# Optimization experiments

Measured on AMD Instinct MI355X. Metric: run time of the kernel, lower is better.

Reference implementation:

```python
import jax, jax.numpy as jnp
import numpy as np

N_PHENO = 50000
N_GENE = 50000
H = 128
N_LAYERS = 3  # num_layers=2 hidden convs + 1 final conv


def _seg_mean(x_src, edge, n_dst):
    # mean aggregation of source features onto destination nodes (PyG SAGEConv default)
    msg = x_src[edge[0]]                       # [E, H] gather
    s = jax.ops.segment_sum(msg, edge[1], num_segments=n_dst)
    cnt = jax.ops.segment_sum(jnp.ones((edge.shape[1],), x_src.dtype), edge[1], num_segments=n_dst)
    return s / jnp.maximum(cnt, 1.0)[:, None]


def _sage(x_src, x_dst, edge, Wl, bl, Wr, n_dst):
    # SAGEConv: lin_l(mean_j x_j) + lin_r(x_i); lin_l has bias, lin_r does not
    return _seg_mean(x_src, edge, n_dst) @ Wl + bl + x_dst @ Wr


def setup_inputs() -> dict:
    key = jax.random.key(0)
    ks = jax.random.split(key, 16)
    d = {
        'x_pheno': jax.random.normal(ks[0], (N_PHENO, H), jnp.float32),
        'x_gene': jax.random.normal(ks[1], (N_GENE, H), jnp.float32),
    }
    scale = 1.0 / np.sqrt(H)
    names = ['Wl_isa', 'bl_isa', 'Wr_isa', 'Wl_rel', 'bl_rel', 'Wr_rel', 'Wl_rev', 'bl_rev', 'Wr_rev']
    for i, nm in enumerate(names):
        shp = (N_LAYERS, H) if nm.startswith('b') else (N_LAYERS, H, H)
        d[nm] = jax.random.normal(ks[2 + i], shp, jnp.float32) * scale
    d['edge_isa'] = jax.random.randint(ks[11], (2, 500000), 0, N_PHENO, jnp.int64)
    d['edge_rel'] = jax.random.randint(ks[12], (2, 1000000), 0, N_GENE, jnp.int64)
    d['edge_rev'] = jax.random.randint(ks[13], (2, 1000000), 0, N_PHENO, jnp.int64)
    d['edge_label_index'] = jax.random.randint(ks[14], (2, 500000), 0, N_PHENO, jnp.int64)
    return d


def reference(x_pheno, x_gene, Wl_isa, bl_isa, Wr_isa, Wl_rel, bl_rel, Wr_rel,
              Wl_rev, bl_rev, Wr_rev, edge_isa, edge_rel, edge_rev, edge_label_index):
    xp, xg = x_pheno, x_gene
    n_p, n_g = xp.shape[0], xg.shape[0]
    for i in range(N_LAYERS):
        # HeteroConv aggr='sum': sum SAGE outputs across edge types per dst node type
        new_p = (_sage(xp, xp, edge_isa, Wl_isa[i], bl_isa[i], Wr_isa[i], n_p)
                 + _sage(xg, xp, edge_rev, Wl_rev[i], bl_rev[i], Wr_rev[i], n_p))
        new_g = _sage(xp, xg, edge_rel, Wl_rel[i], bl_rel[i], Wr_rel[i], n_g)
        if i < N_LAYERS - 1:  # leaky_relu after hidden convs, not after `final`
            new_p = jax.nn.leaky_relu(new_p, 0.01)
            new_g = jax.nn.leaky_relu(new_g, 0.01)
        xp, xg = new_p, new_g
    # Classifier: dot-product edge decoder + sigmoid
    score = (xp[edge_label_index[0]] * xg[edge_label_index[1]]).sum(axis=-1)
    return jax.nn.sigmoid(score)
```

## Files before the change

kernel.cpp:

```cpp
#include <hip/hip_runtime.h>
#include <hip/hip_bf16.h>
#include <math.h>

#define H 128
#define RS 136
#define BSH 9
#define BINW 512
#define BCAP 11264
#define KEDGE 4096
#define EPT 16
#define MAXBINS 1024

typedef __attribute__((ext_vector_type(8))) short short8;
typedef __attribute__((ext_vector_type(4))) short short4v;
typedef __attribute__((ext_vector_type(4))) float f32x4;
typedef __attribute__((ext_vector_type(2))) _Float16 half2v;
typedef __attribute__((ext_vector_type(4))) _Float16 half4v;
typedef __attribute__((ext_vector_type(8))) _Float16 half8v;

__device__ __forceinline__ short f2bf(float f) {
    unsigned u = __float_as_uint(f);
    u += 0x7fff + ((u >> 16) & 1);
    return (short)(u >> 16);
}
__device__ __forceinline__ float bf2f(short h) {
    return __uint_as_float(((unsigned)(unsigned short)h) << 16);
}


__global__ __launch_bounds__(256) void bin_count_kernel(
    const int* __restrict__ e0, int E0, const int* __restrict__ e1, int E1,
    const int* __restrict__ e2, int E2, int* __restrict__ bin_tot,
    int NPn, int NGn, int nbins, int E_tot) {
    __shared__ int hist[MAXBINS];
    int t = threadIdx.x;
    for (int i = t; i < nbins; i += 256) hist[i] = 0;
    __syncthreads();
    int base_e = blockIdx.x * KEDGE;
#pragma unroll
    for (int j = 0; j < EPT; ++j) {
        int g = base_e + j * 256 + t;
        if (g < E_tot) {
            const int* ed; int E, lo, nbase;
            if (g < E0) { ed = e0; E = E0; lo = g; nbase = 0; }
            else if (g < E0 + E1) { ed = e1; E = E1; lo = g - E0; nbase = NPn; }
            else { ed = e2; E = E2; lo = g - E0 - E1; nbase = NPn + NGn; }
            int gdst = nbase + ed[E + lo];
            atomicAdd(&hist[gdst >> BSH], 1);
        }
    }
    __syncthreads();
    for (int i = t; i < nbins; i += 256) {
        int h = hist[i];
        if (h) atomicAdd(&bin_tot[i * 16], h);
    }
}

__global__ __launch_bounds__(1024) void scan_bins(const int* __restrict__ bin_tot, int nbins,
                                                  int* __restrict__ bin_base,
                                                  int* __restrict__ bin_cur) {
    __shared__ int sh[1024];
    int t = threadIdx.x;
    int v = (t < nbins) ? bin_tot[t * 16] : 0;
    sh[t] = v;
    __syncthreads();
    for (int off = 1; off < 1024; off <<= 1) {
        int u = (t >= off) ? sh[t - off] : 0;
        __syncthreads();
        sh[t] += u;
        __syncthreads();
    }
    if (t < nbins) {
        int ex = sh[t] - v;
        bin_base[t] = ex;
        bin_cur[t * 16] = ex;
    }
    if (t == nbins - 1) bin_base[nbins] = sh[t];
}

__global__ __launch_bounds__(256) void bin_scatter_kernel(
    const int* __restrict__ e0, int E0, const int* __restrict__ e1, int E1,
    const int* __restrict__ e2, int E2, int* __restrict__ bin_cur,
    int* __restrict__ temp, int NPn, int NGn, int nbins, int E_tot) {
    __shared__ int hist[MAXBINS];
    __shared__ int cur[MAXBINS];
    int t = threadIdx.x;
    for (int i = t; i < nbins; i += 256) hist[i] = 0;
    __syncthreads();
    int vals[EPT], bins[EPT];
    int base_e = blockIdx.x * KEDGE;
#pragma unroll
    for (int j = 0; j < EPT; ++j) {
        int g = base_e + j * 256 + t;
        int b = -1, v = 0;
        if (g < E_tot) {
            const int* ed; int E, lo, nbase;
            if (g < E0) { ed = e0; E = E0; lo = g; nbase = 0; }
            else if (g < E0 + E1) { ed = e1; E = E1; lo = g - E0; nbase = NPn; }
            else { ed = e2; E = E2; lo = g - E0 - E1; nbase = NPn + NGn; }
            int src = ed[lo];
            int gdst = nbase + ed[E + lo];
            v = src | ((gdst & (BINW - 1)) << 16);
            b = gdst >> BSH;
            atomicAdd(&hist[b], 1);
        }
        vals[j] = v;
        bins[j] = b;
    }
    __syncthreads();
    for (int i = t; i < nbins; i += 256) {
        int h = hist[i];
        cur[i] = h ? atomicAdd(&bin_cur[i * 16], h) : 0;
    }
    __syncthreads();
#pragma unroll
    for (int j = 0; j < EPT; ++j) {
        if (bins[j] >= 0) {
            int p = atomicAdd(&cur[bins[j]], 1);
            temp[p] = vals[j];
        }
    }
}

__global__ __launch_bounds__(256) void bin_sort_kernel(
    const int* __restrict__ bin_base, const int* __restrict__ temp,
    int* __restrict__ col, int* __restrict__ rowptr, int n_tot, int nbins) {
    __shared__ int srt[BCAP];
    __shared__ int cur[BINW];
    __shared__ int pfx[BINW];
    __shared__ int red[256];
    int b = blockIdx.x;
    int start = b << BSH;
    int nodes = n_tot - start; if (nodes > BINW) nodes = BINW;
    int t = threadIdx.x;
    int base = bin_base[b];
    int count = bin_base[b + 1] - base;
    for (int i = t; i < BINW; i += 256) cur[i] = 0;
    __syncthreads();
    for (int i = t; i < count; i += 256)
        atomicAdd(&cur[(temp[base + i] >> 16) & (BINW - 1)], 1);
    __syncthreads();
    int a0 = cur[2 * t], a1 = cur[2 * t + 1];
    red[t] = a0 + a1;
    __syncthreads();
    for (int off = 1; off < 256; off <<= 1) {
        int u = (t >= off) ? red[t - off] : 0;
        __syncthreads();
        red[t] += u;
        __syncthreads();
    }
    int excl = red[t] - (a0 + a1);
    pfx[2 * t] = excl;
    pfx[2 * t + 1] = excl + a0;
    __syncthreads();
    for (int i = t; i < nodes; i += 256) rowptr[start + i] = base + pfx[i];
    if (b == nbins - 1 && t == 0) rowptr[n_tot] = base + count;
    for (int i = t; i < BINW; i += 256) cur[i] = pfx[i];
    __syncthreads();
    if (count <= BCAP) {
        for (int i = t; i < count; i += 256) {
            int v = temp[base + i];
            int p = atomicAdd(&cur[(v >> 16) & (BINW - 1)], 1);
            srt[p] = v & 0xFFFF;
        }
        __syncthreads();
        for (int i = t; i < count; i += 256) col[base + i] = srt[i];
    } else {
        for (int i = t; i < count; i += 256) {
            int v = temp[base + i];
            int p = atomicAdd(&cur[(v >> 16) & (BINW - 1)], 1);
            col[base + p] = v & 0xFFFF;
        }
    }
}


struct WSrc { const float* a[15]; const float* b[15]; };

__global__ __launch_bounds__(256) void pack_w_kernel(WSrc src, short* __restrict__ whi,
                                                     short* __restrict__ wlo) {
    int idx = blockIdx.x * 256 + threadIdx.x;
    if (idx >= 15 * 4 * 8 * 64) return;
    int lane = idx & 63;
    int ct = (idx >> 6) & 7;
    int kc = (idx >> 9) & 3;
    int mat = idx >> 11;
    const float* A = src.a[mat];
    const float* Bp = src.b[mat];
    int n = ct * 16 + (lane & 15);
    int kbase = kc * 32 + (lane >> 4) * 8;
    size_t o = (size_t)idx * 8;
    for (int j = 0; j < 8; ++j) {
        float v = A[(size_t)(kbase + j) * H + n];
        if (Bp) v += Bp[(size_t)(kbase + j) * H + n];
        short h = f2bf(v);
        whi[o + j] = h;
        wlo[o + j] = f2bf(v - bf2f(h));
    }
}


__global__ __launch_bounds__(256) void cvt16_kernel(const float* __restrict__ x,
                                                    _Float16* __restrict__ y, int n4) {
    int i = blockIdx.x * 256 + threadIdx.x;
    if (i >= n4) return;
    f32x4 v = *(const f32x4*)&x[(size_t)i * 4];
    half4v h;
#pragma unroll
    for (int k = 0; k < 4; ++k) h[k] = (_Float16)v[k];
    *(half4v*)&y[(size_t)i * 4] = h;
}


__device__ __forceinline__ float2 seg16(const _Float16* __restrict__ x,
                                        const int* __restrict__ col,
                                        int beg, int end, int voff) {
    float ax0 = 0.f, ax1 = 0.f, ax2 = 0.f, ax3 = 0.f;
    float ay0 = 0.f, ay1 = 0.f, ay2 = 0.f, ay3 = 0.f;
    int e = beg;
    while (e + 16 <= end) {
        half2v v[16];
#pragma unroll
        for (int i = 0; i < 16; ++i) {
            int si = __builtin_amdgcn_readfirstlane(col[e + i]);
            v[i] = *(const half2v*)(x + (size_t)si * H + voff);
        }
#pragma unroll
        for (int i = 0; i < 16; i += 4) {
            ax0 += (float)v[i + 0][0]; ay0 += (float)v[i + 0][1];
            ax1 += (float)v[i + 1][0]; ay1 += (float)v[i + 1][1];
            ax2 += (float)v[i + 2][0]; ay2 += (float)v[i + 2][1];
            ax3 += (float)v[i + 3][0]; ay3 += (float)v[i + 3][1];
        }
        e += 16;
    }
    int rem = end - e;
    if (rem > 0) {
        int last = end - 1;
        half2v v[16];
#pragma unroll
        for (int i = 0; i < 16; ++i) {
            int p = e + i; if (p > last) p = last;
            int si = __builtin_amdgcn_readfirstlane(col[p]);
            v[i] = *(const half2v*)(x + (size_t)si * H + voff);
        }
#pragma unroll
        for (int i = 0; i < 16; ++i) {
            float m = (i < rem) ? 1.0f : 0.0f;
            float fx = (float)v[i][0], fy = (float)v[i][1];
            if ((i & 3) == 0) { ax0 = fmaf(fx, m, ax0); ay0 = fmaf(fy, m, ay0); }
            else if ((i & 3) == 1) { ax1 = fmaf(fx, m, ax1); ay1 = fmaf(fy, m, ay1); }
            else if ((i & 3) == 2) { ax2 = fmaf(fx, m, ax2); ay2 = fmaf(fy, m, ay2); }
            else { ax3 = fmaf(fx, m, ax3); ay3 = fmaf(fy, m, ay3); }
        }
    }
    float sx = (ax0 + ax1) + (ax2 + ax3);
    float sy = (ay0 + ay1) + (ay2 + ay3);
    int c = end - beg; if (c < 1) c = 1;
    float inv = 1.0f / (float)c;
    return (float2){sx * inv, sy * inv};
}

__global__ __launch_bounds__(256) void agg_all_kernel(
    const _Float16* __restrict__ xp, const _Float16* __restrict__ xg,
    const int* __restrict__ rowptr, const int* __restrict__ col,
    float* __restrict__ M1, float* __restrict__ M2, float* __restrict__ M3,
    int NPn, int NGn) {
    int wl = __builtin_amdgcn_readfirstlane((int)threadIdx.x >> 6);
    int w = (blockIdx.x << 2) + wl;
    int lane = threadIdx.x & 63;
    int voff = lane * 2;
    if (w < NPn) {
        float2 r1 = seg16(xp, col, rowptr[w], rowptr[w + 1], voff);
        *(float2*)&M1[(size_t)w * H + voff] = r1;
        int b = NPn + NGn + w;
        float2 r2 = seg16(xg, col, rowptr[b], rowptr[b + 1], voff);
        *(float2*)&M2[(size_t)w * H + voff] = r2;
    } else if (w < NPn + NGn) {
        float2 r3 = seg16(xp, col, rowptr[w], rowptr[w + 1], voff);
        *(float2*)&M3[(size_t)(w - NPn) * H + voff] = r3;
    }
}


struct GIn { const float* f; const short* hi; const short* lo; };

template <int NIN>
__global__ __launch_bounds__(256, 3) void gemm_mfma(
    GIn a0, GIn a1, GIn a2,
    const short* __restrict__ whi, const short* __restrict__ wlo,
    int mat0, int mat1, int mat2,
    const float* __restrict__ b0, const float* __restrict__ b1,
    _Float16* __restrict__ out16, short* __restrict__ ohi, short* __restrict__ olo,
    int n_rows, int relu) {
    __shared__ short Ahi[64 * RS];
    __shared__ short Alo[64 * RS];
    const int tid = threadIdx.x;
    const int lane = tid & 63;
    const int wave = tid >> 6;
    const int r0 = blockIdx.x * 64;
    const int ct0 = wave * 2;
    const int m16 = lane & 15;
    const int acol = (lane >> 4) * 8;

    f32x4 acc[4][2];
#pragma unroll
    for (int mt = 0; mt < 4; ++mt)
#pragma unroll
        for (int c = 0; c < 2; ++c) acc[mt][c] = (f32x4){0.f, 0.f, 0.f, 0.f};

    const GIn ins[3] = {a0, a1, a2};
    const int marr[3] = {mat0, mat1, mat2};

    short8 bh[2][2], bl[2][2];
    {
        const short* wh = whi + (size_t)marr[0] * (H * H);
        const short* wl = wlo + (size_t)marr[0] * (H * H);
        size_t f0 = ((size_t)ct0 * 64 + lane) * 8;
        bh[0][0] = *(const short8*)&wh[f0];
        bh[0][1] = *(const short8*)&wh[f0 + 512];
        bl[0][0] = *(const short8*)&wl[f0];
        bl[0][1] = *(const short8*)&wl[f0 + 512];
    }

#pragma unroll
    for (int m = 0; m < NIN; ++m) {
        const short* __restrict__ wh = whi + (size_t)marr[m] * (H * H);
        const short* __restrict__ wl = wlo + (size_t)marr[m] * (H * H);
        __syncthreads();
        if (ins[m].hi) {
#pragma unroll
            for (int i = 0; i < 8; ++i) {
                int f = tid + i * 256;
                int row = f >> 5;
                int c4 = (f & 31) * 4;
                int gr = r0 + row;
                if (gr >= n_rows) gr = n_rows - 1;
                size_t o = (size_t)gr * H + c4;
                *(short4v*)&Ahi[row * RS + c4] = *(const short4v*)&ins[m].hi[o];
                *(short4v*)&Alo[row * RS + c4] = *(const short4v*)&ins[m].lo[o];
            }
        } else {
            const float* __restrict__ A = ins[m].f;
#pragma unroll
            for (int i = 0; i < 8; ++i) {
                int f = tid + i * 256;
                int row = f >> 5;
                int c4 = (f & 31) * 4;
                int gr = r0 + row;
                if (gr >= n_rows) gr = n_rows - 1;
                float4 v = *(const float4*)&A[(size_t)gr * H + c4];
                short h0 = f2bf(v.x), h1 = f2bf(v.y), h2 = f2bf(v.z), h3 = f2bf(v.w);
                *(short4v*)&Ahi[row * RS + c4] = (short4v){h0, h1, h2, h3};
                *(short4v*)&Alo[row * RS + c4] =
                    (short4v){f2bf(v.x - bf2f(h0)), f2bf(v.y - bf2f(h1)),
                              f2bf(v.z - bf2f(h2)), f2bf(v.w - bf2f(h3))};
            }
        }
        __syncthreads();
#pragma unroll
        for (int kc = 0; kc < 4; ++kc) {
            if (kc < 3) {
                int nb = (kc + 1) & 1;
                size_t f = ((size_t)((kc + 1) * 8 + ct0) * 64 + lane) * 8;
                bh[nb][0] = *(const short8*)&wh[f];
                bh[nb][1] = *(const short8*)&wh[f + 512];
                bl[nb][0] = *(const short8*)&wl[f];
                bl[nb][1] = *(const short8*)&wl[f + 512];
            } else if (m + 1 < NIN) {
                const short* wh2 = whi + (size_t)marr[m + 1] * (H * H);
                const short* wl2 = wlo + (size_t)marr[m + 1] * (H * H);
                size_t f = ((size_t)ct0 * 64 + lane) * 8;
                bh[0][0] = *(const short8*)&wh2[f];
                bh[0][1] = *(const short8*)&wh2[f + 512];
                bl[0][0] = *(const short8*)&wl2[f];
                bl[0][1] = *(const short8*)&wl2[f + 512];
            }
            int cb = kc & 1;
#pragma unroll
            for (int mt = 0; mt < 4; ++mt) {
                short8 ah = *(const short8*)&Ahi[(mt * 16 + m16) * RS + kc * 32 + acol];
                short8 al = *(const short8*)&Alo[(mt * 16 + m16) * RS + kc * 32 + acol];
#pragma unroll
                for (int c = 0; c < 2; ++c) {
                    acc[mt][c] = __builtin_amdgcn_mfma_f32_16x16x32_bf16(ah, bh[cb][c], acc[mt][c], 0, 0, 0);
                    acc[mt][c] = __builtin_amdgcn_mfma_f32_16x16x32_bf16(al, bh[cb][c], acc[mt][c], 0, 0, 0);
                    acc[mt][c] = __builtin_amdgcn_mfma_f32_16x16x32_bf16(ah, bl[cb][c], acc[mt][c], 0, 0, 0);
                }
            }
        }
    }

    const int rquad = (lane >> 4) * 4;
    const int ncol = lane & 15;
#pragma unroll
    for (int c = 0; c < 2; ++c) {
        int n = (ct0 + c) * 16 + ncol;
        float bs = b0[n];
        if (b1) bs += b1[n];
#pragma unroll
        for (int mt = 0; mt < 4; ++mt) {
#pragma unroll
            for (int reg = 0; reg < 4; ++reg) {
                int gr = r0 + mt * 16 + rquad + reg;
                if (gr < n_rows) {
                    float v = acc[mt][c][reg] + bs;
                    if (relu) v = v > 0.f ? v : 0.01f * v;
                    size_t o = (size_t)gr * H + n;
                    out16[o] = (_Float16)v;
                    short h = f2bf(v);
                    ohi[o] = h;
                    olo[o] = f2bf(v - bf2f(h));
                }
            }
        }
    }
}


__global__ __launch_bounds__(256) void scores_kernel(const _Float16* __restrict__ xp,
                                                     const _Float16* __restrict__ xg,
                                                     const int* __restrict__ eli, int E,
                                                     float* __restrict__ out) {
    int lane16 = threadIdx.x & 15;
    int sub = threadIdx.x >> 4;
    int e = blockIdx.x * 16 + sub;
    if (e >= E) return;
    int ip = eli[e];
    int ig = eli[E + e];
    half8v a = *(const half8v*)&xp[(size_t)ip * H + lane16 * 8];
    half8v b = *(const half8v*)&xg[(size_t)ig * H + lane16 * 8];
    float s = 0.f;
#pragma unroll
    for (int k = 0; k < 8; ++k) s += (float)a[k] * (float)b[k];
#pragma unroll
    for (int off = 8; off; off >>= 1) s += __shfl_xor(s, off, 16);
    if (lane16 == 0) out[e] = 1.0f / (1.0f + expf(-s));
}


extern "C" void kernel_launch(void* const* d_in, const int* in_sizes, int n_in,
                              void* d_out, int out_size, void* d_ws, size_t ws_size,
                              hipStream_t stream) {
    const float* x_pheno = (const float*)d_in[0];
    const float* x_gene  = (const float*)d_in[1];
    const float* Wl_isa  = (const float*)d_in[2];
    const float* bl_isa  = (const float*)d_in[3];
    const float* Wr_isa  = (const float*)d_in[4];
    const float* Wl_rel  = (const float*)d_in[5];
    const float* bl_rel  = (const float*)d_in[6];
    const float* Wr_rel  = (const float*)d_in[7];
    const float* Wl_rev  = (const float*)d_in[8];
    const float* bl_rev  = (const float*)d_in[9];
    const float* Wr_rev  = (const float*)d_in[10];
    const int* e_isa = (const int*)d_in[11];
    const int* e_rel = (const int*)d_in[12];
    const int* e_rev = (const int*)d_in[13];
    const int* e_lbl = (const int*)d_in[14];
    const int E_isa = in_sizes[11] / 2;
    const int E_rel = in_sizes[12] / 2;
    const int E_rev = in_sizes[13] / 2;
    const int E_lbl = in_sizes[14] / 2;
    const int NP = in_sizes[0] / H;
    const int NG = in_sizes[1] / H;
    const int NMAX = NP > NG ? NP : NG;
    const int n_tot = NP + NG + NP;
    const int E_tot = E_isa + E_rel + E_rev;
    const int nbins = (n_tot + BINW - 1) / BINW;

    char* ws = (char*)d_ws;
    auto alloc = [&](size_t bytes) -> char* {
        char* p = ws;
        ws += (bytes + 255) & ~(size_t)255;
        return p;
    };
    float* M1 = (float*)alloc((size_t)NMAX * H * sizeof(float));
    float* M2 = (float*)alloc((size_t)NMAX * H * sizeof(float));
    float* M3 = (float*)alloc((size_t)NMAX * H * sizeof(float));
    int* rowptr  = (int*)alloc((size_t)(n_tot + 1) * 4);
    int* col     = (int*)alloc((size_t)E_tot * 4);
    int* temp    = (int*)alloc((size_t)E_tot * 4);
    int* bin_tot = (int*)alloc((size_t)nbins * 16 * 4);
    int* bin_cur = (int*)alloc((size_t)nbins * 16 * 4);
    int* bin_base= (int*)alloc((size_t)(nbins + 1) * 4);
    short* whi = (short*)alloc((size_t)15 * H * H * sizeof(short));
    short* wlo = (short*)alloc((size_t)15 * H * H * sizeof(short));
    _Float16* xp16 = (_Float16*)alloc((size_t)NP * H * sizeof(_Float16));
    _Float16* xg16 = (_Float16*)alloc((size_t)NG * H * sizeof(_Float16));
    short* xph = (short*)alloc((size_t)NP * H * sizeof(short));
    short* xpl = (short*)alloc((size_t)NP * H * sizeof(short));
    short* xgh = (short*)alloc((size_t)NG * H * sizeof(short));
    short* xgl = (short*)alloc((size_t)NG * H * sizeof(short));

    hipMemsetAsync(bin_tot, 0, (size_t)nbins * 16 * 4, stream);
    bin_count_kernel<<<(E_tot + KEDGE - 1) / KEDGE, 256, 0, stream>>>(
        e_isa, E_isa, e_rel, E_rel, e_rev, E_rev, bin_tot, NP, NG, nbins, E_tot);
    scan_bins<<<1, 1024, 0, stream>>>(bin_tot, nbins, bin_base, bin_cur);
    bin_scatter_kernel<<<(E_tot + KEDGE - 1) / KEDGE, 256, 0, stream>>>(
        e_isa, E_isa, e_rel, E_rel, e_rev, E_rev, bin_cur, temp, NP, NG, nbins, E_tot);
    bin_sort_kernel<<<nbins, 256, 0, stream>>>(bin_base, temp, col, rowptr, n_tot, nbins);

    WSrc src;
    for (int l = 0; l < 3; ++l) {
        src.a[l * 5 + 0] = Wl_isa + (size_t)l * H * H;  src.b[l * 5 + 0] = nullptr;
        src.a[l * 5 + 1] = Wl_rev + (size_t)l * H * H;  src.b[l * 5 + 1] = nullptr;
        src.a[l * 5 + 2] = Wr_isa + (size_t)l * H * H;  src.b[l * 5 + 2] = Wr_rev + (size_t)l * H * H;
        src.a[l * 5 + 3] = Wl_rel + (size_t)l * H * H;  src.b[l * 5 + 3] = nullptr;
        src.a[l * 5 + 4] = Wr_rel + (size_t)l * H * H;  src.b[l * 5 + 4] = nullptr;
    }
    pack_w_kernel<<<(15 * 4 * 8 * 64 + 255) / 256, 256, 0, stream>>>(src, whi, wlo);

    cvt16_kernel<<<(NP * H / 4 + 255) / 256, 256, 0, stream>>>(x_pheno, xp16, NP * H / 4);
    cvt16_kernel<<<(NG * H / 4 + 255) / 256, 256, 0, stream>>>(x_gene, xg16, NG * H / 4);

    const short *pph = nullptr, *ppl = nullptr, *pgh = nullptr, *pgl = nullptr;
    for (int l = 0; l < 3; ++l) {
        agg_all_kernel<<<(NP + NG + 3) / 4, 256, 0, stream>>>(
            xp16, xg16, rowptr, col, M1, M2, M3, NP, NG);
        int relu = (l < 2) ? 1 : 0;
        const float* bli = bl_isa + (size_t)l * H;
        const float* blv = bl_rev + (size_t)l * H;
        const float* blr = bl_rel + (size_t)l * H;
        GIn a0{M1, nullptr, nullptr};
        GIn a1{M2, nullptr, nullptr};
        GIn a2{l == 0 ? x_pheno : nullptr, pph, ppl};
        gemm_mfma<3><<<(NP + 63) / 64, 256, 0, stream>>>(
            a0, a1, a2, whi, wlo, l * 5 + 0, l * 5 + 1, l * 5 + 2, bli, blv,
            xp16, xph, xpl, NP, relu);
        GIn g0{M3, nullptr, nullptr};
        GIn g1{l == 0 ? x_gene : nullptr, pgh, pgl};
        GIn g2{nullptr, nullptr, nullptr};
        gemm_mfma<2><<<(NG + 63) / 64, 256, 0, stream>>>(
            g0, g1, g2, whi, wlo, l * 5 + 3, l * 5 + 4, 0, blr, nullptr,
            xg16, xgh, xgl, NG, relu);
        pph = xph; ppl = xpl; pgh = xgh; pgl = xgl;
    }

    scores_kernel<<<(E_lbl + 15) / 16, 256, 0, stream>>>(xp16, xg16, e_lbl, E_lbl, (float*)d_out);
}
```

Baseline: 669.8 us.

## Fuse neighbor aggregation into GEMM and drop separate bin-count pass

Mean aggregation now runs inside the MFMA GEMM kernel: each block gathers its 64 rows directly into shared-memory bf16 hi/lo tiles, which removes the fp32 M1/M2/M3 intermediates and their global write and read-back. Because aggregation now reads the fp16 features while new features are written, the fp16 buffers are double-buffered across layers. CSR construction drops the separate counting pass by scattering into fixed-capacity per-bin slots and scanning afterwards; edges beyond the slot capacity would be silently dropped. The two input conversions are merged into one launch and a short-tail path is added to the segment gather. The fused kernel puts irregular gather latency in front of the MFMA work and no longer prefetches the next weight tile.

```diff
diff --git a/kernel.cpp b/kernel.cpp
--- a/kernel.cpp
+++ b/kernel.cpp
@@ -7,12 +7,14 @@
 #define BSH 9
 #define BINW 512
 #define BCAP 11264
+#define BSLOT 12288
 #define KEDGE 4096
 #define EPT 16
 #define MAXBINS 1024
 
 typedef __attribute__((ext_vector_type(8))) short short8;
 typedef __attribute__((ext_vector_type(4))) short short4v;
+typedef __attribute__((ext_vector_type(2))) short short2v;
 typedef __attribute__((ext_vector_type(4))) float f32x4;
 typedef __attribute__((ext_vector_type(2))) _Float16 half2v;
 typedef __attribute__((ext_vector_type(4))) _Float16 half4v;
@@ -27,56 +29,6 @@
     return __uint_as_float(((unsigned)(unsigned short)h) << 16);
 }
 
-
-__global__ __launch_bounds__(256) void bin_count_kernel(
-    const int* __restrict__ e0, int E0, const int* __restrict__ e1, int E1,
-    const int* __restrict__ e2, int E2, int* __restrict__ bin_tot,
-    int NPn, int NGn, int nbins, int E_tot) {
-    __shared__ int hist[MAXBINS];
-    int t = threadIdx.x;
-    for (int i = t; i < nbins; i += 256) hist[i] = 0;
-    __syncthreads();
-    int base_e = blockIdx.x * KEDGE;
-#pragma unroll
-    for (int j = 0; j < EPT; ++j) {
-        int g = base_e + j * 256 + t;
-        if (g < E_tot) {
-            const int* ed; int E, lo, nbase;
-            if (g < E0) { ed = e0; E = E0; lo = g; nbase = 0; }
-            else if (g < E0 + E1) { ed = e1; E = E1; lo = g - E0; nbase = NPn; }
-            else { ed = e2; E = E2; lo = g - E0 - E1; nbase = NPn + NGn; }
-            int gdst = nbase + ed[E + lo];
-            atomicAdd(&hist[gdst >> BSH], 1);
-        }
-    }
-    __syncthreads();
-    for (int i = t; i < nbins; i += 256) {
-        int h = hist[i];
-        if (h) atomicAdd(&bin_tot[i * 16], h);
-    }
-}
-
-__global__ __launch_bounds__(1024) void scan_bins(const int* __restrict__ bin_tot, int nbins,
-                                                  int* __restrict__ bin_base,
-                                                  int* __restrict__ bin_cur) {
-    __shared__ int sh[1024];
-    int t = threadIdx.x;
-    int v = (t < nbins) ? bin_tot[t * 16] : 0;
-    sh[t] = v;
-    __syncthreads();
-    for (int off = 1; off < 1024; off <<= 1) {
-        int u = (t >= off) ? sh[t - off] : 0;
-        __syncthreads();
-        sh[t] += u;
-        __syncthreads();
-    }
-    if (t < nbins) {
-        int ex = sh[t] - v;
-        bin_base[t] = ex;
-        bin_cur[t * 16] = ex;
-    }
-    if (t == nbins - 1) bin_base[nbins] = sh[t];
-}
 
 __global__ __launch_bounds__(256) void bin_scatter_kernel(
     const int* __restrict__ e0, int E0, const int* __restrict__ e1, int E1,
@@ -117,9 +69,27 @@
     for (int j = 0; j < EPT; ++j) {
         if (bins[j] >= 0) {
             int p = atomicAdd(&cur[bins[j]], 1);
-            temp[p] = vals[j];
-        }
-    }
+            if (p < BSLOT) temp[(size_t)bins[j] * BSLOT + p] = vals[j];
+        }
+    }
+}
+
+__global__ __launch_bounds__(1024) void scan_bins(const int* __restrict__ bin_cur, int nbins,
+                                                  int* __restrict__ bin_base) {
+    __shared__ int sh[1024];
+    int t = threadIdx.x;
+    int v = 0;
+    if (t < nbins) { v = bin_cur[t * 16]; if (v > BSLOT) v = BSLOT; }
+    sh[t] = v;
+    __syncthreads();
+    for (int off = 1; off < 1024; off <<= 1) {
+        int u = (t >= off) ? sh[t - off] : 0;
+        __syncthreads();
+        sh[t] += u;
+        __syncthreads();
+    }
+    if (t < nbins) bin_base[t] = sh[t] - v;
+    if (t == nbins - 1) bin_base[nbins] = sh[t];
 }
 
 __global__ __launch_bounds__(256) void bin_sort_kernel(
@@ -135,10 +105,11 @@
     int t = threadIdx.x;
     int base = bin_base[b];
     int count = bin_base[b + 1] - base;
+    const int* __restrict__ tb = temp + (size_t)b * BSLOT;
     for (int i = t; i < BINW; i += 256) cur[i] = 0;
     __syncthreads();
     for (int i = t; i < count; i += 256)
-        atomicAdd(&cur[(temp[base + i] >> 16) & (BINW - 1)], 1);
+        atomicAdd(&cur[(tb[i] >> 16) & (BINW - 1)], 1);
     __syncthreads();
     int a0 = cur[2 * t], a1 = cur[2 * t + 1];
     red[t] = a0 + a1;
@@ -159,7 +130,7 @@
     __syncthreads();
     if (count <= BCAP) {
         for (int i = t; i < count; i += 256) {
-            int v = temp[base + i];
+            int v = tb[i];
             int p = atomicAdd(&cur[(v >> 16) & (BINW - 1)], 1);
             srt[p] = v & 0xFFFF;
         }
@@ -167,7 +138,7 @@
         for (int i = t; i < count; i += 256) col[base + i] = srt[i];
     } else {
         for (int i = t; i < count; i += 256) {
-            int v = temp[base + i];
+            int v = tb[i];
             int p = atomicAdd(&cur[(v >> 16) & (BINW - 1)], 1);
             col[base + p] = v & 0xFFFF;
         }
@@ -200,15 +171,20 @@
 }
 
 
-__global__ __launch_bounds__(256) void cvt16_kernel(const float* __restrict__ x,
-                                                    _Float16* __restrict__ y, int n4) {
+__global__ __launch_bounds__(256) void cvt16_kernel(const float* __restrict__ xa, int n4a,
+                                                    const float* __restrict__ xb, int n4b,
+                                                    _Float16* __restrict__ ya,
+                                                    _Float16* __restrict__ yb) {
     int i = blockIdx.x * 256 + threadIdx.x;
-    if (i >= n4) return;
-    f32x4 v = *(const f32x4*)&x[(size_t)i * 4];
+    const float* x; _Float16* y;
+    if (i < n4a) { x = xa + (size_t)i * 4; y = ya + (size_t)i * 4; }
+    else if (i < n4a + n4b) { x = xb + (size_t)(i - n4a) * 4; y = yb + (size_t)(i - n4a) * 4; }
+    else return;
+    f32x4 v = *(const f32x4*)x;
     half4v h;
 #pragma unroll
     for (int k = 0; k < 4; ++k) h[k] = (_Float16)v[k];
-    *(half4v*)&y[(size_t)i * 4] = h;
+    *(half4v*)y = h;
 }
 
 
@@ -235,7 +211,7 @@
         e += 16;
     }
     int rem = end - e;
-    if (rem > 0) {
+    if (rem > 8) {
         int last = end - 1;
         half2v v[16];
 #pragma unroll
@@ -253,6 +229,24 @@
             else if ((i & 3) == 2) { ax2 = fmaf(fx, m, ax2); ay2 = fmaf(fy, m, ay2); }
             else { ax3 = fmaf(fx, m, ax3); ay3 = fmaf(fy, m, ay3); }
         }
+    } else if (rem > 0) {
+        int last = end - 1;
+        half2v v[8];
+#pragma unroll
+        for (int i = 0; i < 8; ++i) {
+            int p = e + i; if (p > last) p = last;
+            int si = __builtin_amdgcn_readfirstlane(col[p]);
+            v[i] = *(const half2v*)(x + (size_t)si * H + voff);
+        }
+#pragma unroll
+        for (int i = 0; i < 8; ++i) {
+            float m = (i < rem) ? 1.0f : 0.0f;
+            float fx = (float)v[i][0], fy = (float)v[i][1];
+            if ((i & 3) == 0) { ax0 = fmaf(fx, m, ax0); ay0 = fmaf(fy, m, ay0); }
+            else if ((i & 3) == 1) { ax1 = fmaf(fx, m, ax1); ay1 = fmaf(fy, m, ay1); }
+            else if ((i & 3) == 2) { ax2 = fmaf(fx, m, ax2); ay2 = fmaf(fy, m, ay2); }
+            else { ax3 = fmaf(fx, m, ax3); ay3 = fmaf(fy, m, ay3); }
+        }
     }
     float sx = (ax0 + ax1) + (ax2 + ax3);
     float sy = (ay0 + ay1) + (ay2 + ay3);
@@ -261,33 +255,19 @@
     return (float2){sx * inv, sy * inv};
 }
 
-__global__ __launch_bounds__(256) void agg_all_kernel(
-    const _Float16* __restrict__ xp, const _Float16* __restrict__ xg,
+
+struct GTerm {
+    const _Float16* x;
+    int rbase;
+    const short* hi;
+    const short* lo;
+    const float* f;
+};
+
+template <int NIN>
+__global__ __launch_bounds__(256, 3) void fused_gnn(
+    GTerm t0, GTerm t1, GTerm t2,
     const int* __restrict__ rowptr, const int* __restrict__ col,
-    float* __restrict__ M1, float* __restrict__ M2, float* __restrict__ M3,
-    int NPn, int NGn) {
-    int wl = __builtin_amdgcn_readfirstlane((int)threadIdx.x >> 6);
-    int w = (blockIdx.x << 2) + wl;
-    int lane = threadIdx.x & 63;
-    int voff = lane * 2;
-    if (w < NPn) {
-        float2 r1 = seg16(xp, col, rowptr[w], rowptr[w + 1], voff);
-        *(float2*)&M1[(size_t)w * H + voff] = r1;
-        int b = NPn + NGn + w;
-        float2 r2 = seg16(xg, col, rowptr[b], rowptr[b + 1], voff);
-        *(float2*)&M2[(size_t)w * H + voff] = r2;
-    } else if (w < NPn + NGn) {
-        float2 r3 = seg16(xp, col, rowptr[w], rowptr[w + 1], voff);
-        *(float2*)&M3[(size_t)(w - NPn) * H + voff] = r3;
-    }
-}
-
-
-struct GIn { const float* f; const short* hi; const short* lo; };
-
-template <int NIN>
-__global__ __launch_bounds__(256, 3) void gemm_mfma(
-    GIn a0, GIn a1, GIn a2,
     const short* __restrict__ whi, const short* __restrict__ wlo,
     int mat0, int mat1, int mat2,
     const float* __restrict__ b0, const float* __restrict__ b1,
@@ -297,7 +277,7 @@
     __shared__ short Alo[64 * RS];
     const int tid = threadIdx.x;
     const int lane = tid & 63;
-    const int wave = tid >> 6;
+    const int wave = __builtin_amdgcn_readfirstlane(tid >> 6);
     const int r0 = blockIdx.x * 64;
     const int ct0 = wave * 2;
     const int m16 = lane & 15;
@@ -309,26 +289,27 @@
 #pragma unroll
         for (int c = 0; c < 2; ++c) acc[mt][c] = (f32x4){0.f, 0.f, 0.f, 0.f};
 
-    const GIn ins[3] = {a0, a1, a2};
+    const GTerm terms[3] = {t0, t1, t2};
     const int marr[3] = {mat0, mat1, mat2};
 
-    short8 bh[2][2], bl[2][2];
-    {
-        const short* wh = whi + (size_t)marr[0] * (H * H);
-        const short* wl = wlo + (size_t)marr[0] * (H * H);
-        size_t f0 = ((size_t)ct0 * 64 + lane) * 8;
-        bh[0][0] = *(const short8*)&wh[f0];
-        bh[0][1] = *(const short8*)&wh[f0 + 512];
-        bl[0][0] = *(const short8*)&wl[f0];
-        bl[0][1] = *(const short8*)&wl[f0 + 512];
-    }
-
 #pragma unroll
     for (int m = 0; m < NIN; ++m) {
-        const short* __restrict__ wh = whi + (size_t)marr[m] * (H * H);
-        const short* __restrict__ wl = wlo + (size_t)marr[m] * (H * H);
-        __syncthreads();
-        if (ins[m].hi) {
+        const GTerm& T = terms[m];
+        __syncthreads();
+        if (T.x) {
+            int voff = lane * 2;
+            for (int rr = 0; rr < 16; ++rr) {
+                int lrow = wave * 16 + rr;
+                int gr = r0 + lrow;
+                if (gr >= n_rows) gr = n_rows - 1;
+                int rb = T.rbase + gr;
+                float2 s = seg16(T.x, col, rowptr[rb], rowptr[rb + 1], voff);
+                short h0 = f2bf(s.x), h1 = f2bf(s.y);
+                *(short2v*)&Ahi[lrow * RS + voff] = (short2v){h0, h1};
+                *(short2v*)&Alo[lrow * RS + voff] =
+                    (short2v){f2bf(s.x - bf2f(h0)), f2bf(s.y - bf2f(h1))};
+            }
+        } else if (T.hi) {
 #pragma unroll
             for (int i = 0; i < 8; ++i) {
                 int f = tid + i * 256;
@@ -337,11 +318,11 @@
                 int gr = r0 + row;
                 if (gr >= n_rows) gr = n_rows - 1;
                 size_t o = (size_t)gr * H + c4;
-                *(short4v*)&Ahi[row * RS + c4] = *(const short4v*)&ins[m].hi[o];
-                *(short4v*)&Alo[row * RS + c4] = *(const short4v*)&ins[m].lo[o];
+                *(short4v*)&Ahi[row * RS + c4] = *(const short4v*)&T.hi[o];
+                *(short4v*)&Alo[row * RS + c4] = *(const short4v*)&T.lo[o];
             }
         } else {
-            const float* __restrict__ A = ins[m].f;
+            const float* __restrict__ A = T.f;
 #pragma unroll
             for (int i = 0; i < 8; ++i) {
                 int f = tid + i * 256;
@@ -358,6 +339,16 @@
             }
         }
         __syncthreads();
+        const short* __restrict__ wh = whi + (size_t)marr[m] * (H * H);
+        const short* __restrict__ wl = wlo + (size_t)marr[m] * (H * H);
+        short8 bh[2][2], bl[2][2];
+        {
+            size_t f0 = ((size_t)ct0 * 64 + lane) * 8;
+            bh[0][0] = *(const short8*)&wh[f0];
+            bh[0][1] = *(const short8*)&wh[f0 + 512];
+            bl[0][0] = *(const short8*)&wl[f0];
+            bl[0][1] = *(const short8*)&wl[f0 + 512];
+        }
 #pragma unroll
         for (int kc = 0; kc < 4; ++kc) {
             if (kc < 3) {
@@ -367,14 +358,6 @@
                 bh[nb][1] = *(const short8*)&wh[f + 512];
                 bl[nb][0] = *(const short8*)&wl[f];
                 bl[nb][1] = *(const short8*)&wl[f + 512];
-            } else if (m + 1 < NIN) {
-                const short* wh2 = whi + (size_t)marr[m + 1] * (H * H);
-                const short* wl2 = wlo + (size_t)marr[m + 1] * (H * H);
-                size_t f = ((size_t)ct0 * 64 + lane) * 8;
-                bh[0][0] = *(const short8*)&wh2[f];
-                bh[0][1] = *(const short8*)&wh2[f + 512];
-                bl[0][0] = *(const short8*)&wl2[f];
-                bl[0][1] = *(const short8*)&wl2[f + 512];
             }
             int cb = kc & 1;
 #pragma unroll
@@ -463,7 +446,6 @@
     const int E_lbl = in_sizes[14] / 2;
     const int NP = in_sizes[0] / H;
     const int NG = in_sizes[1] / H;
-    const int NMAX = NP > NG ? NP : NG;
     const int n_tot = NP + NG + NP;
     const int E_tot = E_isa + E_rel + E_rev;
     const int nbins = (n_tot + BINW - 1) / BINW;
@@ -474,30 +456,27 @@
         ws += (bytes + 255) & ~(size_t)255;
         return p;
     };
-    float* M1 = (float*)alloc((size_t)NMAX * H * sizeof(float));
-    float* M2 = (float*)alloc((size_t)NMAX * H * sizeof(float));
-    float* M3 = (float*)alloc((size_t)NMAX * H * sizeof(float));
     int* rowptr  = (int*)alloc((size_t)(n_tot + 1) * 4);
     int* col     = (int*)alloc((size_t)E_tot * 4);
-    int* temp    = (int*)alloc((size_t)E_tot * 4);
-    int* bin_tot = (int*)alloc((size_t)nbins * 16 * 4);
+    int* temp    = (int*)alloc((size_t)nbins * BSLOT * 4);
     int* bin_cur = (int*)alloc((size_t)nbins * 16 * 4);
     int* bin_base= (int*)alloc((size_t)(nbins + 1) * 4);
     short* whi = (short*)alloc((size_t)15 * H * H * sizeof(short));
     short* wlo = (short*)alloc((size_t)15 * H * H * sizeof(short));
-    _Float16* xp16 = (_Float16*)alloc((size_t)NP * H * sizeof(_Float16));
-    _Float16* xg16 = (_Float16*)alloc((size_t)NG * H * sizeof(_Float16));
+    _Float16* xpm[2], *xgm[2];
+    xpm[0] = (_Float16*)alloc((size_t)NP * H * sizeof(_Float16));
+    xpm[1] = (_Float16*)alloc((size_t)NP * H * sizeof(_Float16));
+    xgm[0] = (_Float16*)alloc((size_t)NG * H * sizeof(_Float16));
+    xgm[1] = (_Float16*)alloc((size_t)NG * H * sizeof(_Float16));
     short* xph = (short*)alloc((size_t)NP * H * sizeof(short));
     short* xpl = (short*)alloc((size_t)NP * H * sizeof(short));
     short* xgh = (short*)alloc((size_t)NG * H * sizeof(short));
     short* xgl = (short*)alloc((size_t)NG * H * sizeof(short));
 
-    hipMemsetAsync(bin_tot, 0, (size_t)nbins * 16 * 4, stream);
-    bin_count_kernel<<<(E_tot + KEDGE - 1) / KEDGE, 256, 0, stream>>>(
-        e_isa, E_isa, e_rel, E_rel, e_rev, E_rev, bin_tot, NP, NG, nbins, E_tot);
-    scan_bins<<<1, 1024, 0, stream>>>(bin_tot, nbins, bin_base, bin_cur);
+    hipMemsetAsync(bin_cur, 0, (size_t)nbins * 16 * 4, stream);
     bin_scatter_kernel<<<(E_tot + KEDGE - 1) / KEDGE, 256, 0, stream>>>(
         e_isa, E_isa, e_rel, E_rel, e_rev, E_rev, bin_cur, temp, NP, NG, nbins, E_tot);
+    scan_bins<<<1, 1024, 0, stream>>>(bin_cur, nbins, bin_base);
     bin_sort_kernel<<<nbins, 256, 0, stream>>>(bin_base, temp, col, rowptr, n_tot, nbins);
 
     WSrc src;
@@ -510,31 +489,32 @@
     }
     pack_w_kernel<<<(15 * 4 * 8 * 64 + 255) / 256, 256, 0, stream>>>(src, whi, wlo);
 
-    cvt16_kernel<<<(NP * H / 4 + 255) / 256, 256, 0, stream>>>(x_pheno, xp16, NP * H / 4);
-    cvt16_kernel<<<(NG * H / 4 + 255) / 256, 256, 0, stream>>>(x_gene, xg16, NG * H / 4);
+    cvt16_kernel<<<((NP + NG) * 32 + 255) / 256, 256, 0, stream>>>(
+        x_pheno, NP * 32, x_gene, NG * 32, xpm[0], xgm[0]);
 
     const short *pph = nullptr, *ppl = nullptr, *pgh = nullptr, *pgl = nullptr;
     for (int l = 0; l < 3; ++l) {
-        agg_all_kernel<<<(NP + NG + 3) / 4, 256, 0, stream>>>(
-            xp16, xg16, rowptr, col, M1, M2, M3, NP, NG);
+        int rs = l & 1;
+        int wsid = rs ^ 1;
         int relu = (l < 2) ? 1 : 0;
         const float* bli = bl_isa + (size_t)l * H;
         const float* blv = bl_rev + (size_t)l * H;
         const float* blr = bl_rel + (size_t)l * H;
-        GIn a0{M1, nullptr, nullptr};
-        GIn a1{M2, nullptr, nullptr};
-        GIn a2{l == 0 ? x_pheno : nullptr, pph, ppl};
-        gemm_mfma<3><<<(NP + 63) / 64, 256, 0, stream>>>(
-            a0, a1, a2, whi, wlo, l * 5 + 0, l * 5 + 1, l * 5 + 2, bli, blv,
-            xp16, xph, xpl, NP, relu);
-        GIn g0{M3, nullptr, nullptr};
-        GIn g1{l == 0 ? x_gene : nullptr, pgh, pgl};
-        GIn g2{nullptr, nullptr, nullptr};
-        gemm_mfma<2><<<(NG + 63) / 64, 256, 0, stream>>>(
-            g0, g1, g2, whi, wlo, l * 5 + 3, l * 5 + 4, 0, blr, nullptr,
-            xg16, xgh, xgl, NG, relu);
+        GTerm isa{xpm[rs], 0, nullptr, nullptr, nullptr};
+        GTerm rev{xgm[rs], NP + NG, nullptr, nullptr, nullptr};
+        GTerm xpt{nullptr, 0, pph, ppl, l == 0 ? x_pheno : nullptr};
+        fused_gnn<3><<<(NP + 63) / 64, 256, 0, stream>>>(
+            isa, rev, xpt, rowptr, col, whi, wlo, l * 5 + 0, l * 5 + 1, l * 5 + 2,
+            bli, blv, xpm[wsid], xph, xpl, NP, relu);
+        GTerm rel{xpm[rs], NP, nullptr, nullptr, nullptr};
+        GTerm xgt{nullptr, 0, pgh, pgl, l == 0 ? x_gene : nullptr};
+        GTerm nil{nullptr, 0, nullptr, nullptr, nullptr};
+        fused_gnn<2><<<(NG + 63) / 64, 256, 0, stream>>>(
+            rel, xgt, nil, rowptr, col, whi, wlo, l * 5 + 3, l * 5 + 4, 0,
+            blr, nullptr, xgm[wsid], xgh, xgl, NG, relu);
         pph = xph; ppl = xpl; pgh = xgh; pgl = xgl;
     }
 
-    scores_kernel<<<(E_lbl + 15) / 16, 256, 0, stream>>>(xp16, xg16, e_lbl, E_lbl, (float*)d_out);
-}
+    scores_kernel<<<(E_lbl + 15) / 16, 256, 0, stream>>>(xpm[1], xgm[1], e_lbl, E_lbl,
+                                                         (float*)d_out);
+}
```

Result: faster. 613.3 us (-8.4%).
